# Kernel optimization log

Hardware: AMD Instinct MI355X
Metric: run time of the kernel (lower is better)

The kernel has to match this reference:

```python
import jax, jax.numpy as jnp
import numpy as np

N, H, E, C, V, K = 4096, 256, 128, 32, 64, 20


def setup_inputs() -> dict:
    key = jax.random.key(0)
    ks = jax.random.split(key, 16)
    f = lambda k, s: jax.random.normal(k, s, dtype=jnp.float32)
    return {
        "vec": f(ks[0], (N, H)),
        "inp": f(ks[1], (N, E)),
        "h_prev": f(ks[2], (N, H)),
        "c_prev": f(ks[3], (N, H)),
        "Wlin": f(ks[4], (C, V, H)) * 0.05,
        "blin": f(ks[5], (C, V)) * 0.05,
        "Wec": f(ks[6], (2, H)) * 0.05,
        "bec": f(ks[7], (2,)) * 0.05,
        "Wrel": f(ks[8], (5, H)) * 0.05,
        "brel": f(ks[9], (5,)) * 0.05,
        "W_ih": f(ks[10], (K, 4 * H, E)) * 0.05,
        "b_ih": f(ks[11], (K, 4 * H)) * 0.05,
        "W_hh": f(ks[12], (K, 4 * H, H)) * 0.05,
        "b_hh": f(ks[13], (K, 4 * H)) * 0.05,
        "category": jax.random.randint(ks[14], (N,), 0, C, dtype=jnp.int32),
        "cell_id": jax.random.randint(ks[15], (N,), 0, K, dtype=jnp.int32),
        "true_idx": jax.random.randint(jax.random.fold_in(key, 100), (N,), 0, V, dtype=jnp.int32),
        "ec_idx": jax.random.randint(jax.random.fold_in(key, 101), (N,), 0, 2, dtype=jnp.int32),
        "rel_idx": jax.random.randint(jax.random.fold_in(key, 102), (N,), 0, 5, dtype=jnp.int32),
    }


def _ce(logits, targets):
    # per-row cross entropy (same math as nn.CrossEntropyLoss per example)
    logp = jax.nn.log_softmax(logits, axis=-1)
    return -jnp.take_along_axis(logp, targets[:, None], axis=-1)[:, 0]


def reference(vec, inp, h_prev, c_prev, Wlin, blin, Wec, bec, Wrel, brel,
              W_ih, b_ih, W_hh, b_hh, category, cell_id, true_idx, ec_idx, rel_idx):
    # --- get_log_odds: per-category tiny linear head, selected by category ---
    logits_all = jnp.einsum('nh,cvh->ncv', vec, Wlin) + blin          # [N,C,V]
    logits = jnp.take_along_axis(logits_all, category[:, None, None].astype(jnp.int32), axis=1)[:, 0]  # [N,V]
    logits_ec = vec @ Wec.T + bec                                      # [N,2]
    logits_rel = vec @ Wrel.T + brel                                   # [N,5]

    # --- calculate_loss: CE over valid children + ec + rel ---
    losses = _ce(logits, true_idx) + _ce(logits_ec, ec_idx) + _ce(logits_rel, rel_idx)  # [N]

    # --- get_next: per-child-index LSTMCell, selected by cell_id ---
    gates_all = (jnp.einsum('ne,kge->nkg', inp, W_ih)
                 + jnp.einsum('nh,kgh->nkg', h_prev, W_hh)
                 + b_ih + b_hh)                                        # [N,K,4H]
    gates = jnp.take_along_axis(gates_all, cell_id[:, None, None].astype(jnp.int32), axis=1)[:, 0]  # [N,4H]
    i, f, g, o = jnp.split(gates, 4, axis=-1)                          # torch LSTMCell gate order i,f,g,o
    c_next = jax.nn.sigmoid(f) * c_prev + jax.nn.sigmoid(i) * jnp.tanh(g)
    h_next = jax.nn.sigmoid(o) * jnp.tanh(c_next)

    # pack: [N, 1 + 2H] = loss | h_next | c_next
    return jnp.concatenate([losses[:, None], h_next, c_next], axis=-1)
```

## Files before the change

kernel.cpp:

```cpp
#include <hip/hip_runtime.h>
#include <hip/hip_bf16.h>
#include <math.h>

#define Nn 4096
#define Hdim 256
#define Edim 128
#define Cdim 32
#define Vdim 64
#define Kdim 20
#define G4H 1024
#define OUTS 513

#define NB 8
#define LMAX 160
#define MAXG (NB * LMAX)
#define MAXT2 192
#define PRMAX 4736
#define PR2MAX 5120

#define SEG_A 983040
#define SEG_B 227328
#define SEG_C 163840
#define SEG_D 81920
#define SEG_E 20480
#define SEG_F 2560
#define PACK_T (SEG_A + SEG_B + SEG_C + SEG_D + SEG_E + SEG_F)

typedef short bf16x8 __attribute__((ext_vector_type(8)));
typedef float f32x4 __attribute__((ext_vector_type(4)));

__device__ __forceinline__ float sigmoidf_(float x) { return 1.0f / (1.0f + expf(-x)); }

__device__ __forceinline__ bf16x8 cvt8(float4 f0, float4 f1) {
    bf16x8 r;
    __hip_bfloat16 h;
    h = __float2bfloat16(f0.x); r[0] = *(short*)&h;
    h = __float2bfloat16(f0.y); r[1] = *(short*)&h;
    h = __float2bfloat16(f0.z); r[2] = *(short*)&h;
    h = __float2bfloat16(f0.w); r[3] = *(short*)&h;
    h = __float2bfloat16(f1.x); r[4] = *(short*)&h;
    h = __float2bfloat16(f1.y); r[5] = *(short*)&h;
    h = __float2bfloat16(f1.z); r[6] = *(short*)&h;
    h = __float2bfloat16(f1.w); r[7] = *(short*)&h;
    return r;
}

__device__ __forceinline__ void gl_lds16(const short* g, void* l) {
    __builtin_amdgcn_global_load_lds((const __attribute__((address_space(1))) void*)g,
                                     (__attribute__((address_space(3))) void*)l, 16, 0, 0);
}

__global__ __launch_bounds__(1024) void k_bucket(const int* __restrict__ cell_id,
                                                 const int* __restrict__ category,
                                                 int* __restrict__ pperm, int* __restrict__ pperm2,
                                                 int* __restrict__ tlist, int* __restrict__ tlist2,
                                                 int* __restrict__ meta) {
    __shared__ int cnt[Kdim], cur[Kdim], po[Kdim], tk[Kdim];
    __shared__ int cnt2[Cdim], cur2[Cdim], po2[Cdim], tk2[Cdim];
    int t = threadIdx.x;
    if (t < Kdim) cnt[t] = 0;
    if (t < Cdim) cnt2[t] = 0;
    __syncthreads();
    for (int i = t; i < Nn; i += 1024) {
        atomicAdd(&cnt[cell_id[i]], 1);
        atomicAdd(&cnt2[category[i]], 1);
    }
    __syncthreads();
    if (t == 0) {
        int acc = 0;
        for (int k = 0; k < Kdim; k++) { po[k] = acc; cur[k] = acc; tk[k] = (cnt[k] + 31) >> 5; acc += tk[k] * 32; }
        meta[0] = acc;
        acc = 0;
        for (int m = 0; m < Cdim; m++) { po2[m] = acc; cur2[m] = acc; tk2[m] = (cnt2[m] + 31) >> 5; acc += tk2[m] * 32; }
        meta[1] = acc;
    }
    __syncthreads();
    for (int i = t; i < Nn; i += 1024) {
        int p = atomicAdd(&cur[cell_id[i]], 1);
        pperm[p] = i;
        int p2 = atomicAdd(&cur2[category[i]], 1);
        pperm2[p2] = i;
    }
    for (int i = t; i < MAXG; i += 1024) tlist[3 * i] = -1;
    for (int i = t; i < MAXT2; i += 1024) tlist2[3 * i] = -1;
    __syncthreads();
    for (int i = t; i < (Kdim + Cdim) * 32; i += 1024) {
        if (i < Kdim * 32) {
            int k = i >> 5, j = i & 31;
            int s = cnt[k] + j;
            if (cnt[k] > 0 && s < tk[k] * 32) pperm[po[k] + s] = pperm[po[k]];
        } else {
            int ii = i - Kdim * 32;
            int m = ii >> 5, j = ii & 31;
            int s = cnt2[m] + j;
            if (cnt2[m] > 0 && s < tk2[m] * 32) pperm2[po2[m] + s] = pperm2[po2[m]];
        }
    }
    if (t < Kdim * 4) {
        int u = t, k = u >> 2, hb = u & 3, b = u & 7;
        int base = 0;
        for (int v = b; v < u; v += NB) base += tk[v >> 2];
        int n = tk[k], c = cnt[k];
        for (int s = 0; s < n; s++) {
            int slot = (base + s) * NB + b;
            if (slot < MAXG) {
                int rc = min(32, c - s * 32);
                tlist[3 * slot + 0] = k;
                tlist[3 * slot + 1] = (po[k] >> 5) + s;
                tlist[3 * slot + 2] = (hb * 64) | (rc << 16);
            }
        }
    }
    if (t >= 128 && t < 128 + Cdim) {
        int m = t - 128;
        int base = 0;
        for (int mm = 0; mm < m; mm++) base += tk2[mm];
        int n = tk2[m], c = cnt2[m];
        for (int s = 0; s < n; s++) {
            int slot = base + s;
            if (slot < MAXT2) {
                int rc = min(32, c - s * 32);
                tlist2[3 * slot + 0] = m;
                tlist2[3 * slot + 1] = (po2[m] >> 5) + s;
                tlist2[3 * slot + 2] = rc;
            }
        }
    }
}

__global__ __launch_bounds__(256) void k_pack(
    const float* __restrict__ vec, const float* __restrict__ inp, const float* __restrict__ h_prev,
    const float* __restrict__ Wlin, const float* __restrict__ blin,
    const float* __restrict__ Wec, const float* __restrict__ bec,
    const float* __restrict__ Wrel, const float* __restrict__ brel,
    const float* __restrict__ W_ih, const float* __restrict__ b_ih,
    const float* __restrict__ W_hh, const float* __restrict__ b_hh,
    const int* __restrict__ pperm, const int* __restrict__ pperm2, const int* __restrict__ meta,
    short* __restrict__ Wp, short* __restrict__ Xp, short* __restrict__ Vp, short* __restrict__ Wlp,
    float* __restrict__ bsum, float* __restrict__ bl2)
{
    int tid = blockIdx.x * 256 + threadIdx.x;
    if (tid < SEG_A) {
        int u = tid / 12288;
        int rem = tid % 12288;
        int st = rem / 2048;
        int rem2 = rem % 2048;
        int r = rem2 >> 3, p = rem2 & 7;
        int k = u >> 2, hb = u & 3;
        int c = p ^ (r & 7);
        int kk = st * 64 + c * 8;
        int grow = (r >> 6) * Hdim + hb * 64 + (r & 63);
        const float* src = (kk < Edim) ? W_ih + ((size_t)k * G4H + grow) * Edim + kk
                                       : W_hh + ((size_t)k * G4H + grow) * Hdim + (kk - Edim);
        float4 f0 = *(const float4*)(src);
        float4 f1 = *(const float4*)(src + 4);
        *(bf16x8*)(Wp + ((size_t)(u * 6 + st) * 256 + r) * 64 + p * 8) = cvt8(f0, f1);
    } else if (tid < SEG_A + SEG_B) {
        int t2 = tid - SEG_A;
        int i = t2 / 48;
        int rem = t2 % 48;
        int st = rem >> 3, q = rem & 7;
        if (i < meta[0]) {
            int orig = pperm[i];
            int r = i & 31, pb = i >> 5;
            int c = q ^ (r & 7);
            int kk = st * 64 + c * 8;
            const float* src = (kk < Edim) ? inp + (size_t)orig * Edim + kk
                                           : h_prev + (size_t)orig * Hdim + (kk - Edim);
            float4 f0 = *(const float4*)(src);
            float4 f1 = *(const float4*)(src + 4);
            *(bf16x8*)(Xp + (size_t)pb * 12288 + st * 2048 + r * 64 + q * 8) = cvt8(f0, f1);
        }
    } else if (tid < SEG_A + SEG_B + SEG_C) {
        int t3 = tid - SEG_A - SEG_B;
        int j = t3 / 32;
        int rem = t3 % 32;
        int st = rem >> 3, q = rem & 7;
        if (j < meta[1]) {
            int orig = pperm2[j];
            int r = j & 31, pb2 = j >> 5;
            int c = q ^ (r & 7);
            int kk = st * 64 + c * 8;
            const float* src = vec + (size_t)orig * Hdim + kk;
            float4 f0 = *(const float4*)(src);
            float4 f1 = *(const float4*)(src + 4);
            *(bf16x8*)(Vp + (size_t)pb2 * 8192 + st * 2048 + r * 64 + q * 8) = cvt8(f0, f1);
        }
    } else if (tid < SEG_A + SEG_B + SEG_C + SEG_D) {
        int t4 = tid - SEG_A - SEG_B - SEG_C;
        int m = t4 / 2560;
        int rem = t4 % 2560;
        int st = rem / 640;
        int rem2 = rem % 640;
        int r = rem2 >> 3, q = rem2 & 7;
        int c = q ^ (r & 7);
        int kk = st * 64 + c * 8;
        float4 f0 = {0.f, 0.f, 0.f, 0.f}, f1 = {0.f, 0.f, 0.f, 0.f};
        if (r < 64) {
            const float* src = Wlin + ((size_t)m * Vdim + r) * Hdim + kk;
            f0 = *(const float4*)(src); f1 = *(const float4*)(src + 4);
        } else if (r < 66) {
            const float* src = Wec + (size_t)(r - 64) * Hdim + kk;
            f0 = *(const float4*)(src); f1 = *(const float4*)(src + 4);
        } else if (r < 71) {
            const float* src = Wrel + (size_t)(r - 66) * Hdim + kk;
            f0 = *(const float4*)(src); f1 = *(const float4*)(src + 4);
        }
        *(bf16x8*)(Wlp + (size_t)m * 20480 + st * 5120 + r * 64 + q * 8) = cvt8(f0, f1);
    } else if (tid < SEG_A + SEG_B + SEG_C + SEG_D + SEG_E) {
        int t5 = tid - SEG_A - SEG_B - SEG_C - SEG_D;
        int k = t5 >> 10, rem = t5 & 1023;
        bsum[t5] = b_ih[(size_t)k * G4H + rem] + b_hh[(size_t)k * G4H + rem];
    } else if (tid < PACK_T) {
        int t6 = tid - SEG_A - SEG_B - SEG_C - SEG_D - SEG_E;
        int m = t6 / 80, v = t6 % 80;
        float b = 0.f;
        if (v < 64) b = blin[m * Vdim + v];
        else if (v < 66) b = bec[v - 64];
        else if (v < 71) b = brel[v - 66];
        bl2[t6] = b;
    }
}

__global__ __launch_bounds__(256, 4) void k_main(
    const float* __restrict__ c_prev,
    const short* __restrict__ Wp, const short* __restrict__ Xp,
    const short* __restrict__ Vp, const short* __restrict__ Wlp,
    const float* __restrict__ bsum, const float* __restrict__ bl2,
    const int* __restrict__ pperm, const int* __restrict__ pperm2,
    const int* __restrict__ tlist, const int* __restrict__ tlist2,
    const int* __restrict__ true_idx, const int* __restrict__ ec_idx, const int* __restrict__ rel_idx,
    float* __restrict__ out)
{
    __shared__ __align__(16) char smem[36864];
    int t = threadIdx.x;
    int w = t >> 6, l = t & 63;
    int l15 = l & 15, quad = l >> 4;

    if (blockIdx.x < MAXG) {
        int k = tlist[3 * blockIdx.x];
        if (k < 0) return;
        int pb = tlist[3 * blockIdx.x + 1];
        int e2 = tlist[3 * blockIdx.x + 2];
        int hb0 = e2 & 0xFFFF, rcount = e2 >> 16;
        int u = k * 4 + (hb0 >> 6);

        short* Wbuf = (short*)smem;
        short* Xbuf = (short*)(smem + 32768);

        const short* Wg = Wp + (size_t)u * 6 * 16384;
        const short* Xg = Xp + (size_t)pb * 12288;

        f32x4 acc[2][4];
        #pragma unroll
        for (int m = 0; m < 2; m++)
            #pragma unroll
            for (int g = 0; g < 4; g++)
                acc[m][g] = (f32x4){0.f, 0.f, 0.f, 0.f};

        for (int st = 0; st < 6; st++) {
            __syncthreads();
            #pragma unroll
            for (int j = 0; j < 8; j++)
                gl_lds16(Wg + st * 16384 + (w * 64 + j * 8) * 64 + l * 8,
                         smem + (w * 64 + j * 8) * 128);
            gl_lds16(Xg + st * 2048 + w * 512 + l * 8, smem + 32768 + w * 1024);
            __syncthreads();
            #pragma unroll
            for (int ks = 0; ks < 2; ks++) {
                int p = (ks * 4 + quad) ^ (l15 & 7);
                bf16x8 af[2], bfr[4];
                #pragma unroll
                for (int m = 0; m < 2; m++)
                    af[m] = *(bf16x8*)((char*)Xbuf + (m * 16 + l15) * 128 + p * 16);
                #pragma unroll
                for (int g = 0; g < 4; g++)
                    bfr[g] = *(bf16x8*)((char*)Wbuf + (g * 64 + w * 16 + l15) * 128 + p * 16);
                #pragma unroll
                for (int m = 0; m < 2; m++)
                    #pragma unroll
                    for (int g = 0; g < 4; g++)
                        acc[m][g] = __builtin_amdgcn_mfma_f32_16x16x32_bf16(af[m], bfr[g], acc[m][g], 0, 0, 0);
            }
        }

        int h = hb0 + w * 16 + l15;
        float bs[4];
        #pragma unroll
        for (int g = 0; g < 4; g++)
            bs[g] = bsum[(size_t)k * G4H + g * Hdim + h];

        #pragma unroll
        for (int m = 0; m < 2; m++) {
            #pragma unroll
            for (int reg = 0; reg < 4; reg++) {
                int r = m * 16 + quad * 4 + reg;
                if (r < rcount) {
                    int row = pperm[pb * 32 + r];
                    float iv = acc[m][0][reg] + bs[0];
                    float fv = acc[m][1][reg] + bs[1];
                    float gv = acc[m][2][reg] + bs[2];
                    float ov = acc[m][3][reg] + bs[3];
                    float cp = c_prev[(size_t)row * Hdim + h];
                    float cn = sigmoidf_(fv) * cp + sigmoidf_(iv) * tanhf(gv);
                    float hn = sigmoidf_(ov) * tanhf(cn);
                    out[(size_t)row * OUTS + 1 + h] = hn;
                    out[(size_t)row * OUTS + 1 + Hdim + h] = cn;
                }
            }
        }
    } else {
        int slot = blockIdx.x - MAXG;
        int cm = tlist2[3 * slot];
        if (cm < 0) return;
        int pb2 = tlist2[3 * slot + 1];
        int rcount = tlist2[3 * slot + 2];

        short* Wlbuf = (short*)smem;
        short* Vbuf  = (short*)(smem + 10240);
        float* Lg    = (float*)(smem + 14336);

        const short* Wg = Wlp + (size_t)cm * 20480;
        const short* Vg = Vp + (size_t)pb2 * 8192;

        f32x4 a0[2], a1[2];
        #pragma unroll
        for (int m = 0; m < 2; m++) { a0[m] = (f32x4){0.f,0.f,0.f,0.f}; a1[m] = (f32x4){0.f,0.f,0.f,0.f}; }

        for (int st = 0; st < 4; st++) {
            __syncthreads();
            for (int n = w; n < 10; n += 4)
                gl_lds16(Wg + st * 5120 + n * 512 + l * 8, smem + n * 1024);
            gl_lds16(Vg + st * 2048 + w * 512 + l * 8, smem + 10240 + w * 1024);
            __syncthreads();
            #pragma unroll
            for (int ks = 0; ks < 2; ks++) {
                int p = (ks * 4 + quad) ^ (l15 & 7);
                bf16x8 af[2];
                af[0] = *(bf16x8*)((char*)Vbuf + l15 * 128 + p * 16);
                af[1] = *(bf16x8*)((char*)Vbuf + (16 + l15) * 128 + p * 16);
                bf16x8 b0 = *(bf16x8*)((char*)Wlbuf + (w * 16 + l15) * 128 + p * 16);
                a0[0] = __builtin_amdgcn_mfma_f32_16x16x32_bf16(af[0], b0, a0[0], 0, 0, 0);
                a0[1] = __builtin_amdgcn_mfma_f32_16x16x32_bf16(af[1], b0, a0[1], 0, 0, 0);
                if (w == 3) {
                    bf16x8 b1 = *(bf16x8*)((char*)Wlbuf + (64 + l15) * 128 + p * 16);
                    a1[0] = __builtin_amdgcn_mfma_f32_16x16x32_bf16(af[0], b1, a1[0], 0, 0, 0);
                    a1[1] = __builtin_amdgcn_mfma_f32_16x16x32_bf16(af[1], b1, a1[1], 0, 0, 0);
                }
            }
        }
        __syncthreads();
        {
            int col = w * 16 + l15;
            float bb = bl2[cm * 80 + col];
            #pragma unroll
            for (int m = 0; m < 2; m++)
                #pragma unroll
                for (int reg = 0; reg < 4; reg++)
                    Lg[(m * 16 + quad * 4 + reg) * 84 + col] = a0[m][reg] + bb;
            if (w == 3) {
                int col1 = 64 + l15;
                float bb1 = bl2[cm * 80 + col1];
                #pragma unroll
                for (int m = 0; m < 2; m++)
                    #pragma unroll
                    for (int reg = 0; reg < 4; reg++)
                        Lg[(m * 16 + quad * 4 + reg) * 84 + col1] = a1[m][reg] + bb1;
            }
        }
        __syncthreads();
        for (int rr = 0; rr < 8; rr++) {
            int r = w * 8 + rr;
            if (r >= rcount) break;
            int orig = pperm2[pb2 * 32 + r];
            float lg = Lg[r * 84 + l];
            float mx = lg;
            for (int s = 32; s >= 1; s >>= 1) mx = fmaxf(mx, __shfl_xor(mx, s));
            float sm = expf(lg - mx);
            for (int s = 32; s >= 1; s >>= 1) sm += __shfl_xor(sm, s);
            float lt = __shfl(lg, true_idx[orig]);
            float loss = mx + logf(sm) - lt;
            if (l == 0) {
                float l0 = Lg[r * 84 + 64], l1 = Lg[r * 84 + 65];
                float me = fmaxf(l0, l1);
                loss += me + logf(expf(l0 - me) + expf(l1 - me)) - ((ec_idx[orig] == 0) ? l0 : l1);
                float rl[5] = { Lg[r * 84 + 66], Lg[r * 84 + 67], Lg[r * 84 + 68], Lg[r * 84 + 69], Lg[r * 84 + 70] };
                float mr = rl[0];
                #pragma unroll
                for (int i = 1; i < 5; i++) mr = fmaxf(mr, rl[i]);
                float sr = 0.f;
                #pragma unroll
                for (int i = 0; i < 5; i++) sr += expf(rl[i] - mr);
                loss += mr + logf(sr) - rl[rel_idx[orig]];
                out[(size_t)orig * OUTS] = loss;
            }
        }
    }
}

extern "C" void kernel_launch(void* const* d_in, const int* in_sizes, int n_in,
                              void* d_out, int out_size, void* d_ws, size_t ws_size,
                              hipStream_t stream) {
    const float* vec      = (const float*)d_in[0];
    const float* inp      = (const float*)d_in[1];
    const float* h_prev   = (const float*)d_in[2];
    const float* c_prev   = (const float*)d_in[3];
    const float* Wlin     = (const float*)d_in[4];
    const float* blin     = (const float*)d_in[5];
    const float* Wec      = (const float*)d_in[6];
    const float* bec      = (const float*)d_in[7];
    const float* Wrel     = (const float*)d_in[8];
    const float* brel     = (const float*)d_in[9];
    const float* W_ih     = (const float*)d_in[10];
    const float* b_ih     = (const float*)d_in[11];
    const float* W_hh     = (const float*)d_in[12];
    const float* b_hh     = (const float*)d_in[13];
    const int*   category = (const int*)d_in[14];
    const int*   cell_id  = (const int*)d_in[15];
    const int*   true_idx = (const int*)d_in[16];
    const int*   ec_idx   = (const int*)d_in[17];
    const int*   rel_idx  = (const int*)d_in[18];
    float* out = (float*)d_out;

    char* ws = (char*)d_ws;
    int*   pperm  = (int*)(ws);
    int*   pperm2 = (int*)(ws + 18944);
    int*   tlist  = (int*)(ws + 39424);
    int*   tlist2 = (int*)(ws + 54784);
    int*   meta   = (int*)(ws + 57088);
    short* Wp     = (short*)(ws + 57344);
    short* Xp     = (short*)(ws + 15785984);
    short* Vp     = (short*)(ws + 19423232);
    short* Wlp    = (short*)(ws + 22044672);
    float* bsum   = (float*)(ws + 23355392);
    float* bl2    = (float*)(ws + 23437312);

    k_bucket<<<1, 1024, 0, stream>>>(cell_id, category, pperm, pperm2, tlist, tlist2, meta);

    k_pack<<<PACK_T / 256, 256, 0, stream>>>(
        vec, inp, h_prev, Wlin, blin, Wec, bec, Wrel, brel,
        W_ih, b_ih, W_hh, b_hh, pperm, pperm2, meta,
        Wp, Xp, Vp, Wlp, bsum, bl2);

    k_main<<<MAXG + MAXT2, 256, 0, stream>>>(
        c_prev, Wp, Xp, Vp, Wlp, bsum, bl2,
        pperm, pperm2, tlist, tlist2, true_idx, ec_idx, rel_idx, out);
}
```

Measured before the change: 153.6 us.

## Fuse bucketing into pack kernel and gather activations directly in main kernel

Merges the single-block bucketing kernel into the pack kernel as block 0, which removes one launch. The separate staging of permuted bf16 activations (Xp, Vp) is dropped: the main kernel now gathers rows of inp/h_prev/vec through a shared-memory row index, converts them to bf16 and writes them straight into LDS. This saves a global write/read round trip for activations and a kernel boundary. In exchange, the main kernel uses synchronous register loads instead of async global_load_lds for X, and activation rows are re-read and re-converted by every hb/weight tile that uses them.

Result: slower. 162.2 us (+5.6%).

```diff
diff --git a/kernel.cpp b/kernel.cpp
--- a/kernel.cpp
+++ b/kernel.cpp
@@ -15,16 +15,12 @@
 #define LMAX 160
 #define MAXG (NB * LMAX)
 #define MAXT2 192
-#define PRMAX 4736
-#define PR2MAX 5120
 
 #define SEG_A 983040
-#define SEG_B 227328
-#define SEG_C 163840
 #define SEG_D 81920
 #define SEG_E 20480
 #define SEG_F 2560
-#define PACK_T (SEG_A + SEG_B + SEG_C + SEG_D + SEG_E + SEG_F)
+#define PACK_T (SEG_A + SEG_D + SEG_E + SEG_F)
 
 typedef short bf16x8 __attribute__((ext_vector_type(8)));
 typedef float f32x4 __attribute__((ext_vector_type(4)));
@@ -50,96 +46,94 @@
                                      (__attribute__((address_space(3))) void*)l, 16, 0, 0);
 }
 
-__global__ __launch_bounds__(1024) void k_bucket(const int* __restrict__ cell_id,
-                                                 const int* __restrict__ category,
-                                                 int* __restrict__ pperm, int* __restrict__ pperm2,
-                                                 int* __restrict__ tlist, int* __restrict__ tlist2,
-                                                 int* __restrict__ meta) {
-    __shared__ int cnt[Kdim], cur[Kdim], po[Kdim], tk[Kdim];
-    __shared__ int cnt2[Cdim], cur2[Cdim], po2[Cdim], tk2[Cdim];
-    int t = threadIdx.x;
-    if (t < Kdim) cnt[t] = 0;
-    if (t < Cdim) cnt2[t] = 0;
-    __syncthreads();
-    for (int i = t; i < Nn; i += 1024) {
-        atomicAdd(&cnt[cell_id[i]], 1);
-        atomicAdd(&cnt2[category[i]], 1);
-    }
-    __syncthreads();
-    if (t == 0) {
-        int acc = 0;
-        for (int k = 0; k < Kdim; k++) { po[k] = acc; cur[k] = acc; tk[k] = (cnt[k] + 31) >> 5; acc += tk[k] * 32; }
-        meta[0] = acc;
-        acc = 0;
-        for (int m = 0; m < Cdim; m++) { po2[m] = acc; cur2[m] = acc; tk2[m] = (cnt2[m] + 31) >> 5; acc += tk2[m] * 32; }
-        meta[1] = acc;
-    }
-    __syncthreads();
-    for (int i = t; i < Nn; i += 1024) {
-        int p = atomicAdd(&cur[cell_id[i]], 1);
-        pperm[p] = i;
-        int p2 = atomicAdd(&cur2[category[i]], 1);
-        pperm2[p2] = i;
-    }
-    for (int i = t; i < MAXG; i += 1024) tlist[3 * i] = -1;
-    for (int i = t; i < MAXT2; i += 1024) tlist2[3 * i] = -1;
-    __syncthreads();
-    for (int i = t; i < (Kdim + Cdim) * 32; i += 1024) {
-        if (i < Kdim * 32) {
-            int k = i >> 5, j = i & 31;
-            int s = cnt[k] + j;
-            if (cnt[k] > 0 && s < tk[k] * 32) pperm[po[k] + s] = pperm[po[k]];
-        } else {
-            int ii = i - Kdim * 32;
-            int m = ii >> 5, j = ii & 31;
-            int s = cnt2[m] + j;
-            if (cnt2[m] > 0 && s < tk2[m] * 32) pperm2[po2[m] + s] = pperm2[po2[m]];
-        }
-    }
-    if (t < Kdim * 4) {
-        int u = t, k = u >> 2, hb = u & 3, b = u & 7;
-        int base = 0;
-        for (int v = b; v < u; v += NB) base += tk[v >> 2];
-        int n = tk[k], c = cnt[k];
-        for (int s = 0; s < n; s++) {
-            int slot = (base + s) * NB + b;
-            if (slot < MAXG) {
-                int rc = min(32, c - s * 32);
-                tlist[3 * slot + 0] = k;
-                tlist[3 * slot + 1] = (po[k] >> 5) + s;
-                tlist[3 * slot + 2] = (hb * 64) | (rc << 16);
-            }
-        }
-    }
-    if (t >= 128 && t < 128 + Cdim) {
-        int m = t - 128;
-        int base = 0;
-        for (int mm = 0; mm < m; mm++) base += tk2[mm];
-        int n = tk2[m], c = cnt2[m];
-        for (int s = 0; s < n; s++) {
-            int slot = base + s;
-            if (slot < MAXT2) {
-                int rc = min(32, c - s * 32);
-                tlist2[3 * slot + 0] = m;
-                tlist2[3 * slot + 1] = (po2[m] >> 5) + s;
-                tlist2[3 * slot + 2] = rc;
-            }
-        }
-    }
-}
-
-__global__ __launch_bounds__(256) void k_pack(
-    const float* __restrict__ vec, const float* __restrict__ inp, const float* __restrict__ h_prev,
+__global__ __launch_bounds__(256) void k_prep(
+    const int* __restrict__ cell_id, const int* __restrict__ category,
     const float* __restrict__ Wlin, const float* __restrict__ blin,
     const float* __restrict__ Wec, const float* __restrict__ bec,
     const float* __restrict__ Wrel, const float* __restrict__ brel,
     const float* __restrict__ W_ih, const float* __restrict__ b_ih,
     const float* __restrict__ W_hh, const float* __restrict__ b_hh,
-    const int* __restrict__ pperm, const int* __restrict__ pperm2, const int* __restrict__ meta,
-    short* __restrict__ Wp, short* __restrict__ Xp, short* __restrict__ Vp, short* __restrict__ Wlp,
+    int* __restrict__ pperm, int* __restrict__ pperm2,
+    int* __restrict__ tlist, int* __restrict__ tlist2, int* __restrict__ meta,
+    short* __restrict__ Wp, short* __restrict__ Wlp,
     float* __restrict__ bsum, float* __restrict__ bl2)
 {
-    int tid = blockIdx.x * 256 + threadIdx.x;
+    int t = threadIdx.x;
+    if (blockIdx.x == 0) {
+        __shared__ int cnt[Kdim], cur[Kdim], po[Kdim], tk[Kdim];
+        __shared__ int cnt2[Cdim], cur2[Cdim], po2[Cdim], tk2[Cdim];
+        if (t < Kdim) cnt[t] = 0;
+        if (t < Cdim) cnt2[t] = 0;
+        __syncthreads();
+        for (int i = t; i < Nn; i += 256) {
+            atomicAdd(&cnt[cell_id[i]], 1);
+            atomicAdd(&cnt2[category[i]], 1);
+        }
+        __syncthreads();
+        if (t == 0) {
+            int acc = 0;
+            for (int k = 0; k < Kdim; k++) { po[k] = acc; cur[k] = acc; tk[k] = (cnt[k] + 31) >> 5; acc += tk[k] * 32; }
+            meta[0] = acc;
+            acc = 0;
+            for (int m = 0; m < Cdim; m++) { po2[m] = acc; cur2[m] = acc; tk2[m] = (cnt2[m] + 31) >> 5; acc += tk2[m] * 32; }
+            meta[1] = acc;
+        }
+        __syncthreads();
+        for (int i = t; i < Nn; i += 256) {
+            int p = atomicAdd(&cur[cell_id[i]], 1);
+            pperm[p] = i;
+            int p2 = atomicAdd(&cur2[category[i]], 1);
+            pperm2[p2] = i;
+        }
+        for (int i = t; i < MAXG; i += 256) tlist[3 * i] = -1;
+        if (t < MAXT2) tlist2[3 * t] = -1;
+        __syncthreads();
+        for (int i = t; i < (Kdim + Cdim) * 32; i += 256) {
+            if (i < Kdim * 32) {
+                int k = i >> 5, j = i & 31;
+                int s = cnt[k] + j;
+                if (cnt[k] > 0 && s < tk[k] * 32) pperm[po[k] + s] = pperm[po[k]];
+            } else {
+                int ii = i - Kdim * 32;
+                int m = ii >> 5, j = ii & 31;
+                int s = cnt2[m] + j;
+                if (cnt2[m] > 0 && s < tk2[m] * 32) pperm2[po2[m] + s] = pperm2[po2[m]];
+            }
+        }
+        if (t < Kdim * 4) {
+            int u = t, k = u >> 2, hb = u & 3, b = u & 7;
+            int base = 0;
+            for (int v = b; v < u; v += NB) base += tk[v >> 2];
+            int n = tk[k], c = cnt[k];
+            for (int s = 0; s < n; s++) {
+                int slot = (base + s) * NB + b;
+                if (slot < MAXG) {
+                    int rc = min(32, c - s * 32);
+                    tlist[3 * slot + 0] = k;
+                    tlist[3 * slot + 1] = (po[k] >> 5) + s;
+                    tlist[3 * slot + 2] = (hb * 64) | (rc << 16);
+                }
+            }
+        }
+        if (t >= 128 && t < 128 + Cdim) {
+            int m = t - 128;
+            int base = 0;
+            for (int mm = 0; mm < m; mm++) base += tk2[mm];
+            int n = tk2[m], c = cnt2[m];
+            for (int s = 0; s < n; s++) {
+                int slot = base + s;
+                if (slot < MAXT2) {
+                    int rc = min(32, c - s * 32);
+                    tlist2[3 * slot + 0] = m;
+                    tlist2[3 * slot + 1] = (po2[m] >> 5) + s;
+                    tlist2[3 * slot + 2] = rc;
+                }
+            }
+        }
+        return;
+    }
+
+    int tid = (blockIdx.x - 1) * 256 + t;
     if (tid < SEG_A) {
         int u = tid / 12288;
         int rem = tid % 12288;
@@ -155,39 +149,8 @@
         float4 f0 = *(const float4*)(src);
         float4 f1 = *(const float4*)(src + 4);
         *(bf16x8*)(Wp + ((size_t)(u * 6 + st) * 256 + r) * 64 + p * 8) = cvt8(f0, f1);
-    } else if (tid < SEG_A + SEG_B) {
-        int t2 = tid - SEG_A;
-        int i = t2 / 48;
-        int rem = t2 % 48;
-        int st = rem >> 3, q = rem & 7;
-        if (i < meta[0]) {
-            int orig = pperm[i];
-            int r = i & 31, pb = i >> 5;
-            int c = q ^ (r & 7);
-            int kk = st * 64 + c * 8;
-            const float* src = (kk < Edim) ? inp + (size_t)orig * Edim + kk
-                                           : h_prev + (size_t)orig * Hdim + (kk - Edim);
-            float4 f0 = *(const float4*)(src);
-            float4 f1 = *(const float4*)(src + 4);
-            *(bf16x8*)(Xp + (size_t)pb * 12288 + st * 2048 + r * 64 + q * 8) = cvt8(f0, f1);
-        }
-    } else if (tid < SEG_A + SEG_B + SEG_C) {
-        int t3 = tid - SEG_A - SEG_B;
-        int j = t3 / 32;
-        int rem = t3 % 32;
-        int st = rem >> 3, q = rem & 7;
-        if (j < meta[1]) {
-            int orig = pperm2[j];
-            int r = j & 31, pb2 = j >> 5;
-            int c = q ^ (r & 7);
-            int kk = st * 64 + c * 8;
-            const float* src = vec + (size_t)orig * Hdim + kk;
-            float4 f0 = *(const float4*)(src);
-            float4 f1 = *(const float4*)(src + 4);
-            *(bf16x8*)(Vp + (size_t)pb2 * 8192 + st * 2048 + r * 64 + q * 8) = cvt8(f0, f1);
-        }
-    } else if (tid < SEG_A + SEG_B + SEG_C + SEG_D) {
-        int t4 = tid - SEG_A - SEG_B - SEG_C;
+    } else if (tid < SEG_A + SEG_D) {
+        int t4 = tid - SEG_A;
         int m = t4 / 2560;
         int rem = t4 % 2560;
         int st = rem / 640;
@@ -207,12 +170,12 @@
             f0 = *(const float4*)(src); f1 = *(const float4*)(src + 4);
         }
         *(bf16x8*)(Wlp + (size_t)m * 20480 + st * 5120 + r * 64 + q * 8) = cvt8(f0, f1);
-    } else if (tid < SEG_A + SEG_B + SEG_C + SEG_D + SEG_E) {
-        int t5 = tid - SEG_A - SEG_B - SEG_C - SEG_D;
+    } else if (tid < SEG_A + SEG_D + SEG_E) {
+        int t5 = tid - SEG_A - SEG_D;
         int k = t5 >> 10, rem = t5 & 1023;
         bsum[t5] = b_ih[(size_t)k * G4H + rem] + b_hh[(size_t)k * G4H + rem];
     } else if (tid < PACK_T) {
-        int t6 = tid - SEG_A - SEG_B - SEG_C - SEG_D - SEG_E;
+        int t6 = tid - SEG_A - SEG_D - SEG_E;
         int m = t6 / 80, v = t6 % 80;
         float b = 0.f;
         if (v < 64) b = blin[m * Vdim + v];
@@ -223,16 +186,16 @@
 }
 
 __global__ __launch_bounds__(256, 4) void k_main(
-    const float* __restrict__ c_prev,
-    const short* __restrict__ Wp, const short* __restrict__ Xp,
-    const short* __restrict__ Vp, const short* __restrict__ Wlp,
+    const float* __restrict__ inp, const float* __restrict__ h_prev,
+    const float* __restrict__ c_prev, const float* __restrict__ vec,
+    const short* __restrict__ Wp, const short* __restrict__ Wlp,
     const float* __restrict__ bsum, const float* __restrict__ bl2,
     const int* __restrict__ pperm, const int* __restrict__ pperm2,
     const int* __restrict__ tlist, const int* __restrict__ tlist2,
     const int* __restrict__ true_idx, const int* __restrict__ ec_idx, const int* __restrict__ rel_idx,
     float* __restrict__ out)
 {
-    __shared__ __align__(16) char smem[36864];
+    __shared__ __align__(16) char smem[36992];
     int t = threadIdx.x;
     int w = t >> 6, l = t & 63;
     int l15 = l & 15, quad = l >> 4;
@@ -247,9 +210,15 @@
 
         short* Wbuf = (short*)smem;
         short* Xbuf = (short*)(smem + 32768);
+        int* rows_s = (int*)(smem + 36864);
+
+        if (t < 32) rows_s[t] = pperm[pb * 32 + t];
 
         const short* Wg = Wp + (size_t)u * 6 * 16384;
-        const short* Xg = Xp + (size_t)pb * 12288;
+
+        int rs = w * 8 + (l >> 3);
+        int q = l & 7;
+        int cc = q ^ (rs & 7);
 
         f32x4 acc[2][4];
         #pragma unroll
@@ -264,7 +233,15 @@
             for (int j = 0; j < 8; j++)
                 gl_lds16(Wg + st * 16384 + (w * 64 + j * 8) * 64 + l * 8,
                          smem + (w * 64 + j * 8) * 128);
-            gl_lds16(Xg + st * 2048 + w * 512 + l * 8, smem + 32768 + w * 1024);
+            {
+                int kk = st * 64 + cc * 8;
+                int row = rows_s[rs];
+                const float* src = (kk < Edim) ? inp + (size_t)row * Edim + kk
+                                               : h_prev + (size_t)row * Hdim + (kk - Edim);
+                float4 f0 = *(const float4*)(src);
+                float4 f1 = *(const float4*)(src + 4);
+                *(bf16x8*)(smem + 32768 + rs * 128 + q * 16) = cvt8(f0, f1);
+            }
             __syncthreads();
             #pragma unroll
             for (int ks = 0; ks < 2; ks++) {
@@ -296,7 +273,7 @@
             for (int reg = 0; reg < 4; reg++) {
                 int r = m * 16 + quad * 4 + reg;
                 if (r < rcount) {
-                    int row = pperm[pb * 32 + r];
+                    int row = rows_s[r];
                     float iv = acc[m][0][reg] + bs[0];
                     float fv = acc[m][1][reg] + bs[1];
                     float gv = acc[m][2][reg] + bs[2];
@@ -319,9 +296,15 @@
         short* Wlbuf = (short*)smem;
         short* Vbuf  = (short*)(smem + 10240);
         float* Lg    = (float*)(smem + 14336);
+        int* rows2_s = (int*)(smem + 36864);
+
+        if (t < 32) rows2_s[t] = pperm2[pb2 * 32 + t];
 
         const short* Wg = Wlp + (size_t)cm * 20480;
-        const short* Vg = Vp + (size_t)pb2 * 8192;
+
+        int rs = w * 8 + (l >> 3);
+        int q = l & 7;
+        int cc = q ^ (rs & 7);
 
         f32x4 a0[2], a1[2];
         #pragma unroll
@@ -331,7 +314,14 @@
             __syncthreads();
             for (int n = w; n < 10; n += 4)
                 gl_lds16(Wg + st * 5120 + n * 512 + l * 8, smem + n * 1024);
-            gl_lds16(Vg + st * 2048 + w * 512 + l * 8, smem + 10240 + w * 1024);
+            {
+                int kk = st * 64 + cc * 8;
+                int row = rows2_s[rs];
+                const float* src = vec + (size_t)row * Hdim + kk;
+                float4 f0 = *(const float4*)(src);
+                float4 f1 = *(const float4*)(src + 4);
+                *(bf16x8*)(smem + 10240 + rs * 128 + q * 16) = cvt8(f0, f1);
+            }
             __syncthreads();
             #pragma unroll
             for (int ks = 0; ks < 2; ks++) {
@@ -372,7 +362,7 @@
         for (int rr = 0; rr < 8; rr++) {
             int r = w * 8 + rr;
             if (r >= rcount) break;
-            int orig = pperm2[pb2 * 32 + r];
+            int orig = rows2_s[r];
             float lg = Lg[r * 84 + l];
             float mx = lg;
             for (int s = 32; s >= 1; s >>= 1) mx = fmaxf(mx, __shfl_xor(mx, s));
@@ -429,20 +419,16 @@
     int*   tlist2 = (int*)(ws + 54784);
     int*   meta   = (int*)(ws + 57088);
     short* Wp     = (short*)(ws + 57344);
-    short* Xp     = (short*)(ws + 15785984);
-    short* Vp     = (short*)(ws + 19423232);
-    short* Wlp    = (short*)(ws + 22044672);
-    float* bsum   = (float*)(ws + 23355392);
-    float* bl2    = (float*)(ws + 23437312);
-
-    k_bucket<<<1, 1024, 0, stream>>>(cell_id, category, pperm, pperm2, tlist, tlist2, meta);
-
-    k_pack<<<PACK_T / 256, 256, 0, stream>>>(
-        vec, inp, h_prev, Wlin, blin, Wec, bec, Wrel, brel,
-        W_ih, b_ih, W_hh, b_hh, pperm, pperm2, meta,
-        Wp, Xp, Vp, Wlp, bsum, bl2);
+    short* Wlp    = (short*)(ws + 15785984);
+    float* bsum   = (float*)(ws + 17096704);
+    float* bl2    = (float*)(ws + 17178624);
+
+    k_prep<<<1 + PACK_T / 256, 256, 0, stream>>>(
+        cell_id, category, Wlin, blin, Wec, bec, Wrel, brel,
+        W_ih, b_ih, W_hh, b_hh,
+        pperm, pperm2, tlist, tlist2, meta, Wp, Wlp, bsum, bl2);
 
     k_main<<<MAXG + MAXT2, 256, 0, stream>>>(
-        c_prev, Wp, Xp, Vp, Wlp, bsum, bl2,
+        inp, h_prev, c_prev, vec, Wp, Wlp, bsum, bl2,
         pperm, pperm2, tlist, tlist2, true_idx, ec_idx, rel_idx, out);
 }
```
